# Kernel tuning notes

Measured on AMD Instinct MI355X. Metric: run time of the kernel, lower is better.

The kernel has to match this reference:

```python
import jax, jax.numpy as jnp
import numpy as np

N = 100000
E = 1200000
F_IN = 128
HID = 32
HEADS = 4
OUT_HEADS = 1
N_CLASSES = 40
NEG_SLOPE = 0.2


def _glorot(key, shape):
    fan_in, fan_out = shape[0], shape[-1]
    lim = jnp.sqrt(6.0 / (fan_in + fan_out))
    return jax.random.uniform(key, shape, jnp.float32, -lim, lim)


def setup_inputs() -> dict:
    key = jax.random.key(0)
    ks = jax.random.split(key, 16)
    x = jax.random.normal(ks[0], (N, F_IN), jnp.float32)
    edge_index = jax.random.randint(ks[1], (2, E), 0, N, jnp.int32)
    # layer 0: F_IN -> HID per head, HEADS heads, concat
    W0 = _glorot(ks[2], (F_IN, HEADS * HID))
    a_src0 = _glorot(ks[3], (HEADS, HID))
    a_dst0 = _glorot(ks[4], (HEADS, HID))
    b0 = jnp.zeros((HEADS * HID,), jnp.float32)
    # layer 1: HEADS*HID -> HID per head, HEADS heads, concat
    W1 = _glorot(ks[5], (HEADS * HID, HEADS * HID))
    a_src1 = _glorot(ks[6], (HEADS, HID))
    a_dst1 = _glorot(ks[7], (HEADS, HID))
    b1 = jnp.zeros((HEADS * HID,), jnp.float32)
    # layer 2: HEADS*HID -> N_CLASSES, OUT_HEADS heads, concat=False (mean)
    W2 = _glorot(ks[8], (HEADS * HID, OUT_HEADS * N_CLASSES))
    a_src2 = _glorot(ks[9], (OUT_HEADS, N_CLASSES))
    a_dst2 = _glorot(ks[10], (OUT_HEADS, N_CLASSES))
    b2 = jnp.zeros((N_CLASSES,), jnp.float32)
    return dict(x=x, edge_index=edge_index,
                W0=W0, a_src0=a_src0, a_dst0=a_dst0, b0=b0,
                W1=W1, a_src1=a_src1, a_dst1=a_dst1, b1=b1,
                W2=W2, a_src2=a_src2, a_dst2=a_dst2, b2=b2)


def gat_conv(x, src, dst, W, a_src, a_dst, b, heads, ch, concat):
    n = x.shape[0]
    h = (x @ W).reshape(n, heads, ch)                      # [N,H,C]
    # per-node attention logits for source/target roles
    s_src = jnp.einsum('nhc,hc->nh', h, a_src)             # [N,H]
    s_dst = jnp.einsum('nhc,hc->nh', h, a_dst)             # [N,H]
    e = jax.nn.leaky_relu(s_src[src] + s_dst[dst], NEG_SLOPE)  # [E,H]
    # segment softmax over incoming edges of each target node
    emax = jax.ops.segment_max(e, dst, num_segments=n)
    ex = jnp.exp(e - emax[dst])
    denom = jax.ops.segment_sum(ex, dst, num_segments=n)
    alpha = ex / (denom[dst] + 1e-16)                       # [E,H]
    msg = h[src] * alpha[:, :, None]                        # [E,H,C]
    out = jax.ops.segment_sum(msg, dst, num_segments=n)     # [N,H,C]
    out = out.reshape(n, heads * ch) if concat else out.mean(axis=1)
    return out + b


def reference(x, edge_index, W0, a_src0, a_dst0, b0, W1, a_src1, a_dst1, b1,
              W2, a_src2, a_dst2, b2):
    # add self loops (PyG GATConv default)
    loops = jnp.arange(N, dtype=edge_index.dtype)
    src = jnp.concatenate([edge_index[0], loops])
    dst = jnp.concatenate([edge_index[1], loops])
    h = jax.nn.elu(gat_conv(x, src, dst, W0, a_src0, a_dst0, b0, HEADS, HID, True))
    h = jax.nn.elu(gat_conv(h, src, dst, W1, a_src1, a_dst1, b1, HEADS, HID, True))
    h = gat_conv(h, src, dst, W2, a_src2, a_dst2, b2, OUT_HEADS, N_CLASSES, False)
    return jax.nn.log_softmax(h, axis=1)
```

## Files before the change

kernel.cpp:

```cpp
#include <hip/hip_runtime.h>
#include <hip/hip_bf16.h>

#define FIN   128
#define HEADS 4
#define HID   32
#define NCLS  40
#define NEG_SLOPE 0.2f

#define BKT_SH 10
#define BKT    1024
#define NB_MAX 128
#define TILE_E 4096

typedef __bf16 bf16x8 __attribute__((ext_vector_type(8)));
typedef float  f32x4  __attribute__((ext_vector_type(4)));

__device__ inline unsigned short bf16_rne(float f) {
    unsigned u = __float_as_uint(f);
    return (unsigned short)((u + 0x7fffu + ((u >> 16) & 1u)) >> 16);
}
__device__ inline float bf16_to_f(unsigned short h) {
    return __uint_as_float(((unsigned)h) << 16);
}

template<int NC>
__global__ void packW_k(const float* __restrict__ W, unsigned short* __restrict__ Bhi,
                        unsigned short* __restrict__ Blo, int NO) {
    int idx = blockIdx.x * 256 + threadIdx.x;
    int total = 4 * NC * 64 * 8;
    if (idx >= total) return;
    int i = idx & 7;
    int rest = idx >> 3;
    int l = rest & 63;
    int rest2 = rest >> 6;
    int c = rest2 % NC;
    int t = rest2 / NC;
    int k   = t * 32 + (l >> 4) * 8 + i;
    int col = c * 16 + (l & 15);
    float val = (col < NO) ? W[(size_t)k * NO + col] : 0.f;
    unsigned short hi = bf16_rne(val);
    unsigned short lo = bf16_rne(val - bf16_to_f(hi));
    Bhi[idx] = hi;
    Blo[idx] = lo;
}

template<int HH, int CH>
__global__ void packS_k(const float* __restrict__ W, const float* __restrict__ asrc,
                        const float* __restrict__ adst, unsigned short* __restrict__ Shi,
                        unsigned short* __restrict__ Slo, int NO) {
    int idx = blockIdx.x * 256 + threadIdx.x;
    int total = 4 * 64 * 8;
    if (idx >= total) return;
    int i = idx & 7;
    int l = (idx >> 3) & 63;
    int t = idx >> 9;
    int k = t * 32 + (l >> 4) * 8 + i;
    int j = l & 15;
    float val = 0.f;
    if (j < HH) {
        const float* wr = W + (size_t)k * NO + j * CH;
        const float* av = asrc + j * CH;
        for (int c = 0; c < CH; ++c) val += wr[c] * av[c];
    } else if (j < 2 * HH) {
        int h = j - HH;
        const float* wr = W + (size_t)k * NO + h * CH;
        const float* av = adst + h * CH;
        for (int c = 0; c < CH; ++c) val += wr[c] * av[c];
    }
    unsigned short hi = bf16_rne(val);
    unsigned short lo = bf16_rne(val - bf16_to_f(hi));
    Shi[idx] = hi;
    Slo[idx] = lo;
}

template<int NC, int HH>
__global__ __launch_bounds__(256) void gemm_fused_k(
        const float* __restrict__ X, const unsigned short* __restrict__ Bhi,
        const unsigned short* __restrict__ Blo, const unsigned short* __restrict__ Shi,
        const unsigned short* __restrict__ Slo, unsigned short* __restrict__ Hbf,
        float* __restrict__ ssrc, float* __restrict__ sdst, int n, int NO) {
    int wave = threadIdx.x >> 6;
    int lane = threadIdx.x & 63;
    int rowbase = (blockIdx.x * 4 + wave) * 32;
    if (rowbase >= n) return;
    int r0 = lane & 15, kg = lane >> 4;

    f32x4 acc[2][NC];
    f32x4 accS[2];
#pragma unroll
    for (int rt = 0; rt < 2; ++rt) {
        accS[rt] = f32x4{0.f, 0.f, 0.f, 0.f};
#pragma unroll
        for (int c = 0; c < NC; ++c) acc[rt][c] = f32x4{0.f, 0.f, 0.f, 0.f};
    }

    for (int t = 0; t < 4; ++t) {
        union U { unsigned short u[8]; bf16x8 v; };
        U ah[2], al[2];
#pragma unroll
        for (int rt = 0; rt < 2; ++rt) {
            int row = min(rowbase + rt * 16 + r0, n - 1);
            const float* xp = X + (size_t)row * 128 + t * 32 + kg * 8;
            float4 xa = *reinterpret_cast<const float4*>(xp);
            float4 xb = *reinterpret_cast<const float4*>(xp + 4);
            float f[8] = {xa.x, xa.y, xa.z, xa.w, xb.x, xb.y, xb.z, xb.w};
#pragma unroll
            for (int i = 0; i < 8; ++i) {
                unsigned short h = bf16_rne(f[i]);
                ah[rt].u[i] = h;
                al[rt].u[i] = bf16_rne(f[i] - bf16_to_f(h));
            }
        }
#pragma unroll
        for (int c = 0; c < NC; ++c) {
            size_t boff = (((size_t)t * NC + c) * 64 + lane) * 8;
            bf16x8 bh = *reinterpret_cast<const bf16x8*>(Bhi + boff);
            bf16x8 bl = *reinterpret_cast<const bf16x8*>(Blo + boff);
#pragma unroll
            for (int rt = 0; rt < 2; ++rt) {
                acc[rt][c] = __builtin_amdgcn_mfma_f32_16x16x32_bf16(ah[rt].v, bh, acc[rt][c], 0, 0, 0);
                acc[rt][c] = __builtin_amdgcn_mfma_f32_16x16x32_bf16(al[rt].v, bh, acc[rt][c], 0, 0, 0);
                acc[rt][c] = __builtin_amdgcn_mfma_f32_16x16x32_bf16(ah[rt].v, bl, acc[rt][c], 0, 0, 0);
            }
        }
        {
            size_t soff = ((size_t)t * 64 + lane) * 8;
            bf16x8 sh = *reinterpret_cast<const bf16x8*>(Shi + soff);
            bf16x8 sl = *reinterpret_cast<const bf16x8*>(Slo + soff);
#pragma unroll
            for (int rt = 0; rt < 2; ++rt) {
                accS[rt] = __builtin_amdgcn_mfma_f32_16x16x32_bf16(ah[rt].v, sh, accS[rt], 0, 0, 0);
                accS[rt] = __builtin_amdgcn_mfma_f32_16x16x32_bf16(al[rt].v, sh, accS[rt], 0, 0, 0);
                accS[rt] = __builtin_amdgcn_mfma_f32_16x16x32_bf16(ah[rt].v, sl, accS[rt], 0, 0, 0);
            }
        }
    }

#pragma unroll
    for (int rt = 0; rt < 2; ++rt)
#pragma unroll
        for (int r = 0; r < 4; ++r) {
            int row = rowbase + rt * 16 + kg * 4 + r;
            if (row >= n) continue;
            if (HH == 4) {
                if (r0 < 4)      ssrc[(size_t)row * 4 + r0]       = accS[rt][r];
                else if (r0 < 8) sdst[(size_t)row * 4 + (r0 - 4)] = accS[rt][r];
            } else {
                if (r0 == 0)      ssrc[row] = accS[rt][r];
                else if (r0 == 1) sdst[row] = accS[rt][r];
            }
#pragma unroll
            for (int c = 0; c < NC; ++c) {
                int col = c * 16 + r0;
                if (col < NO)
                    Hbf[(size_t)row * NO + col] = bf16_rne(acc[rt][c][r]);
            }
        }
}

template<int NC, int HH>
__global__ __launch_bounds__(256) void gemm_bf16s_k(
        const unsigned short* __restrict__ Xbf, const unsigned short* __restrict__ Bhi,
        const unsigned short* __restrict__ Blo, const unsigned short* __restrict__ Shi,
        const unsigned short* __restrict__ Slo, unsigned short* __restrict__ Hbf,
        float* __restrict__ ssrc, float* __restrict__ sdst, int n, int NO) {
    int wave = threadIdx.x >> 6;
    int lane = threadIdx.x & 63;
    int rowbase = (blockIdx.x * 4 + wave) * 32;
    if (rowbase >= n) return;
    int r0 = lane & 15, kg = lane >> 4;

    f32x4 acc[2][NC];
    f32x4 accS[2];
#pragma unroll
    for (int rt = 0; rt < 2; ++rt) {
        accS[rt] = f32x4{0.f, 0.f, 0.f, 0.f};
#pragma unroll
        for (int c = 0; c < NC; ++c) acc[rt][c] = f32x4{0.f, 0.f, 0.f, 0.f};
    }

    for (int t = 0; t < 4; ++t) {
        bf16x8 av[2];
#pragma unroll
        for (int rt = 0; rt < 2; ++rt) {
            int row = min(rowbase + rt * 16 + r0, n - 1);
            av[rt] = *reinterpret_cast<const bf16x8*>(Xbf + (size_t)row * 128 + t * 32 + kg * 8);
        }
#pragma unroll
        for (int c = 0; c < NC; ++c) {
            size_t boff = (((size_t)t * NC + c) * 64 + lane) * 8;
            bf16x8 bh = *reinterpret_cast<const bf16x8*>(Bhi + boff);
            bf16x8 bl = *reinterpret_cast<const bf16x8*>(Blo + boff);
#pragma unroll
            for (int rt = 0; rt < 2; ++rt) {
                acc[rt][c] = __builtin_amdgcn_mfma_f32_16x16x32_bf16(av[rt], bh, acc[rt][c], 0, 0, 0);
                acc[rt][c] = __builtin_amdgcn_mfma_f32_16x16x32_bf16(av[rt], bl, acc[rt][c], 0, 0, 0);
            }
        }
        {
            size_t soff = ((size_t)t * 64 + lane) * 8;
            bf16x8 sh = *reinterpret_cast<const bf16x8*>(Shi + soff);
            bf16x8 sl = *reinterpret_cast<const bf16x8*>(Slo + soff);
#pragma unroll
            for (int rt = 0; rt < 2; ++rt) {
                accS[rt] = __builtin_amdgcn_mfma_f32_16x16x32_bf16(av[rt], sh, accS[rt], 0, 0, 0);
                accS[rt] = __builtin_amdgcn_mfma_f32_16x16x32_bf16(av[rt], sl, accS[rt], 0, 0, 0);
            }
        }
    }

#pragma unroll
    for (int rt = 0; rt < 2; ++rt)
#pragma unroll
        for (int r = 0; r < 4; ++r) {
            int row = rowbase + rt * 16 + kg * 4 + r;
            if (row >= n) continue;
            if (HH == 4) {
                if (r0 < 4)      ssrc[(size_t)row * 4 + r0]       = accS[rt][r];
                else if (r0 < 8) sdst[(size_t)row * 4 + (r0 - 4)] = accS[rt][r];
            } else {
                if (r0 == 0)      ssrc[row] = accS[rt][r];
                else if (r0 == 1) sdst[row] = accS[rt][r];
            }
#pragma unroll
            for (int c = 0; c < NC; ++c) {
                int col = c * 16 + r0;
                if (col < NO)
                    Hbf[(size_t)row * NO + col] = bf16_rne(acc[rt][c][r]);
            }
        }
}

__global__ __launch_bounds__(256) void histA_k(const int* __restrict__ ei, int E, int Etot,
                                               int nb, int* __restrict__ cnt1) {
    __shared__ int h[NB_MAX];
    for (int i = threadIdx.x; i < nb; i += 256) h[i] = 0;
    __syncthreads();
    int base = blockIdx.x * TILE_E;
    int lim = min(base + TILE_E, Etot);
    for (int e = base + threadIdx.x; e < lim; e += 256) {
        int d = (e < E) ? ei[E + e] : e - E;
        atomicAdd(&h[d >> BKT_SH], 1);
    }
    __syncthreads();
    for (int i = threadIdx.x; i < nb; i += 256)
        if (h[i]) atomicAdd(&cnt1[i], h[i]);
}

__global__ void scanB_k(const int* __restrict__ cnt1, int* __restrict__ bbase,
                        int* __restrict__ gcur1, int nb) {
    __shared__ int tmp[128];
    int l = threadIdx.x;
    int v = (l < nb) ? cnt1[l] : 0;
    tmp[l] = v;
    __syncthreads();
    for (int off = 1; off < 128; off <<= 1) {
        int t = (l >= off) ? tmp[l - off] : 0;
        __syncthreads();
        tmp[l] += t;
        __syncthreads();
    }
    if (l < nb) { int ex = tmp[l] - v; bbase[l] = ex; gcur1[l] = ex; }
    if (l == 0) bbase[nb] = tmp[127];
}

__global__ __launch_bounds__(256) void placeA_k(const int* __restrict__ ei, int E, int Etot,
                                                int nb, int* __restrict__ gcur1,
                                                unsigned* __restrict__ pairs) {
    __shared__ int h[NB_MAX];
    __shared__ int cur[NB_MAX];
    for (int i = threadIdx.x; i < nb; i += 256) h[i] = 0;
    __syncthreads();
    int base = blockIdx.x * TILE_E;
    int lim = min(base + TILE_E, Etot);
    for (int e = base + threadIdx.x; e < lim; e += 256) {
        int d = (e < E) ? ei[E + e] : e - E;
        atomicAdd(&h[d >> BKT_SH], 1);
    }
    __syncthreads();
    for (int i = threadIdx.x; i < nb; i += 256)
        cur[i] = h[i] ? atomicAdd(&gcur1[i], h[i]) : 0;
    __syncthreads();
    for (int e = base + threadIdx.x; e < lim; e += 256) {
        int s, d;
        if (e < E) { s = ei[e]; d = ei[E + e]; } else { s = d = e - E; }
        int p = atomicAdd(&cur[d >> BKT_SH], 1);
        pairs[p] = ((unsigned)s << BKT_SH) | (unsigned)(d & (BKT - 1));
    }
}

__global__ __launch_bounds__(256) void buildcsr_k(const unsigned* __restrict__ pairs,
                                                  const int* __restrict__ bbase,
                                                  int* __restrict__ rowptr,
                                                  int* __restrict__ cols,
                                                  int n, int etot) {
    __shared__ int cnt[BKT];
    __shared__ int part[256];
    int b = blockIdx.x;
    int d0 = b << BKT_SH;
    int nd = min(BKT, n - d0);
    int rbeg = bbase[b], rend = bbase[b + 1];
    for (int i = threadIdx.x; i < nd; i += 256) cnt[i] = 0;
    __syncthreads();
    for (int i = rbeg + threadIdx.x; i < rend; i += 256)
        atomicAdd(&cnt[pairs[i] & (BKT - 1)], 1);
    __syncthreads();

    int t = threadIdx.x;
    int i4 = t * 4;
    int myv[4];
    int s0 = 0;
#pragma unroll
    for (int j = 0; j < 4; ++j) { myv[j] = (i4 + j < nd) ? cnt[i4 + j] : 0; s0 += myv[j]; }
    part[t] = s0;
    __syncthreads();
    for (int off = 1; off < 256; off <<= 1) {
        int tv = (t >= off) ? part[t - off] : 0;
        __syncthreads();
        part[t] += tv;
        __syncthreads();
    }
    int run = rbeg + part[t] - s0;
#pragma unroll
    for (int j = 0; j < 4; ++j) {
        if (i4 + j < nd) {
            rowptr[d0 + i4 + j] = run;
            cnt[i4 + j] = run;
            run += myv[j];
        }
    }
    if (b == 0 && t == 0) rowptr[n] = etot;
    __syncthreads();
    for (int i = rbeg + threadIdx.x; i < rend; i += 256) {
        unsigned p = pairs[i];
        int pos = atomicAdd(&cnt[p & (BKT - 1)], 1);
        cols[pos] = (int)(p >> BKT_SH);
    }
}

__global__ __launch_bounds__(256) void gat128_k(
        const int* __restrict__ rp, const int* __restrict__ cols,
        const unsigned short* __restrict__ Hbf, const float* __restrict__ ssrc,
        const float* __restrict__ sdst, const float* __restrict__ bias,
        unsigned short* __restrict__ outbf, int n) {
    int d = (blockIdx.x * 256 + threadIdx.x) >> 4;
    if (d >= n) return;
    int l = threadIdx.x & 15;
    int head = l >> 2;
    int sub  = l & 3;
    int beg = rp[d], end = rp[d + 1];

    float sdh = sdst[(size_t)d * 4 + head];

    float m = -1e30f, den = 0.f;
    for (int i = beg + sub; i < end; i += 4) {
        int s = cols[i];
        float v = ssrc[(size_t)s * 4 + head] + sdh;
        v = (v >= 0.f) ? v : NEG_SLOPE * v;
        float nm = fmaxf(m, v);
        den = den * __expf(m - nm) + __expf(v - nm);
        m = nm;
    }
#pragma unroll
    for (int off = 1; off <= 2; off <<= 1) {
        float om = __shfl_xor(m, off, 64);
        float od = __shfl_xor(den, off, 64);
        float nm = fmaxf(m, om);
        den = den * __expf(m - nm) + od * __expf(om - nm);
        m = nm;
    }
    float r = 1.f / (den + 1e-16f);

    float4 a0 = {0.f, 0.f, 0.f, 0.f}, a1 = {0.f, 0.f, 0.f, 0.f};
    float4 c0 = {0.f, 0.f, 0.f, 0.f}, c1 = {0.f, 0.f, 0.f, 0.f};

    auto proc = [&](int i, float4& p0, float4& p1) {
        int s = cols[i];
        float v = ssrc[(size_t)s * 4 + head] + sdh;
        v = (v >= 0.f) ? v : NEG_SLOPE * v;
        float a = __expf(v - m);
        const unsigned short* hp = Hbf + (size_t)s * 128 + l * 8;
        uint4 q = *reinterpret_cast<const uint4*>(hp);
        float f0 = __uint_as_float(q.x << 16);
        float f1 = __uint_as_float(q.x & 0xffff0000u);
        float f2 = __uint_as_float(q.y << 16);
        float f3 = __uint_as_float(q.y & 0xffff0000u);
        float f4 = __uint_as_float(q.z << 16);
        float f5 = __uint_as_float(q.z & 0xffff0000u);
        float f6 = __uint_as_float(q.w << 16);
        float f7 = __uint_as_float(q.w & 0xffff0000u);
        p0.x += a * f0; p0.y += a * f1; p0.z += a * f2; p0.w += a * f3;
        p1.x += a * f4; p1.y += a * f5; p1.z += a * f6; p1.w += a * f7;
    };

    int i = beg;
    int rem = (end - beg) & 3;
    if (rem & 1) { proc(i, a0, a1); ++i; }
    if (rem & 2) { proc(i, a0, a1); proc(i + 1, c0, c1); i += 2; }
    for (; i < end; i += 4) {
        int s0 = cols[i], s1 = cols[i + 1], s2 = cols[i + 2], s3 = cols[i + 3];
        float w0 = ssrc[(size_t)s0 * 4 + head] + sdh;
        float w1 = ssrc[(size_t)s1 * 4 + head] + sdh;
        float w2 = ssrc[(size_t)s2 * 4 + head] + sdh;
        float w3 = ssrc[(size_t)s3 * 4 + head] + sdh;
        uint4 q0 = *reinterpret_cast<const uint4*>(Hbf + (size_t)s0 * 128 + l * 8);
        uint4 q1 = *reinterpret_cast<const uint4*>(Hbf + (size_t)s1 * 128 + l * 8);
        uint4 q2 = *reinterpret_cast<const uint4*>(Hbf + (size_t)s2 * 128 + l * 8);
        uint4 q3 = *reinterpret_cast<const uint4*>(Hbf + (size_t)s3 * 128 + l * 8);
        w0 = (w0 >= 0.f) ? w0 : NEG_SLOPE * w0;
        w1 = (w1 >= 0.f) ? w1 : NEG_SLOPE * w1;
        w2 = (w2 >= 0.f) ? w2 : NEG_SLOPE * w2;
        w3 = (w3 >= 0.f) ? w3 : NEG_SLOPE * w3;
        float e0 = __expf(w0 - m), e1 = __expf(w1 - m);
        float e2 = __expf(w2 - m), e3 = __expf(w3 - m);
        a0.x += e0 * __uint_as_float(q0.x << 16);
        a0.y += e0 * __uint_as_float(q0.x & 0xffff0000u);
        a0.z += e0 * __uint_as_float(q0.y << 16);
        a0.w += e0 * __uint_as_float(q0.y & 0xffff0000u);
        a1.x += e0 * __uint_as_float(q0.z << 16);
        a1.y += e0 * __uint_as_float(q0.z & 0xffff0000u);
        a1.z += e0 * __uint_as_float(q0.w << 16);
        a1.w += e0 * __uint_as_float(q0.w & 0xffff0000u);
        c0.x += e1 * __uint_as_float(q1.x << 16);
        c0.y += e1 * __uint_as_float(q1.x & 0xffff0000u);
        c0.z += e1 * __uint_as_float(q1.y << 16);
        c0.w += e1 * __uint_as_float(q1.y & 0xffff0000u);
        c1.x += e1 * __uint_as_float(q1.z << 16);
        c1.y += e1 * __uint_as_float(q1.z & 0xffff0000u);
        c1.z += e1 * __uint_as_float(q1.w << 16);
        c1.w += e1 * __uint_as_float(q1.w & 0xffff0000u);
        a0.x += e2 * __uint_as_float(q2.x << 16);
        a0.y += e2 * __uint_as_float(q2.x & 0xffff0000u);
        a0.z += e2 * __uint_as_float(q2.y << 16);
        a0.w += e2 * __uint_as_float(q2.y & 0xffff0000u);
        a1.x += e2 * __uint_as_float(q2.z << 16);
        a1.y += e2 * __uint_as_float(q2.z & 0xffff0000u);
        a1.z += e2 * __uint_as_float(q2.w << 16);
        a1.w += e2 * __uint_as_float(q2.w & 0xffff0000u);
        c0.x += e3 * __uint_as_float(q3.x << 16);
        c0.y += e3 * __uint_as_float(q3.x & 0xffff0000u);
        c0.z += e3 * __uint_as_float(q3.y << 16);
        c0.w += e3 * __uint_as_float(q3.y & 0xffff0000u);
        c1.x += e3 * __uint_as_float(q3.z << 16);
        c1.y += e3 * __uint_as_float(q3.z & 0xffff0000u);
        c1.z += e3 * __uint_as_float(q3.w << 16);
        c1.w += e3 * __uint_as_float(q3.w & 0xffff0000u);
    }
    a0.x += c0.x; a0.y += c0.y; a0.z += c0.z; a0.w += c0.w;
    a1.x += c1.x; a1.y += c1.y; a1.z += c1.z; a1.w += c1.w;

    float4 b0 = *reinterpret_cast<const float4*>(bias + l * 8);
    float4 b1 = *reinterpret_cast<const float4*>(bias + l * 8 + 4);
    float4 v0, v1;
    v0.x = a0.x * r + b0.x; v0.y = a0.y * r + b0.y;
    v0.z = a0.z * r + b0.z; v0.w = a0.w * r + b0.w;
    v1.x = a1.x * r + b1.x; v1.y = a1.y * r + b1.y;
    v1.z = a1.z * r + b1.z; v1.w = a1.w * r + b1.w;
    v0.x = (v0.x > 0.f) ? v0.x : expm1f(v0.x);
    v0.y = (v0.y > 0.f) ? v0.y : expm1f(v0.y);
    v0.z = (v0.z > 0.f) ? v0.z : expm1f(v0.z);
    v0.w = (v0.w > 0.f) ? v0.w : expm1f(v0.w);
    v1.x = (v1.x > 0.f) ? v1.x : expm1f(v1.x);
    v1.y = (v1.y > 0.f) ? v1.y : expm1f(v1.y);
    v1.z = (v1.z > 0.f) ? v1.z : expm1f(v1.z);
    v1.w = (v1.w > 0.f) ? v1.w : expm1f(v1.w);

    uint4 u;
    u.x = (unsigned)bf16_rne(v0.x) | ((unsigned)bf16_rne(v0.y) << 16);
    u.y = (unsigned)bf16_rne(v0.z) | ((unsigned)bf16_rne(v0.w) << 16);
    u.z = (unsigned)bf16_rne(v1.x) | ((unsigned)bf16_rne(v1.y) << 16);
    u.w = (unsigned)bf16_rne(v1.z) | ((unsigned)bf16_rne(v1.w) << 16);
    *reinterpret_cast<uint4*>(outbf + (size_t)d * 128 + l * 8) = u;
}

__global__ __launch_bounds__(256) void gat40_k(
        const int* __restrict__ rp, const int* __restrict__ cols,
        const unsigned short* __restrict__ Hbf, const float* __restrict__ ssrc,
        const float* __restrict__ sdst, const float* __restrict__ b2,
        float* __restrict__ out, int n) {
    int d = (blockIdx.x * 256 + threadIdx.x) >> 4;
    if (d >= n) return;
    int l = threadIdx.x & 15;
    int beg = rp[d], end = rp[d + 1];
    float sd = sdst[d];

    float m = -1e30f, den = 0.f;
    for (int i = beg + l; i < end; i += 16) {
        int s = cols[i];
        float v = ssrc[s] + sd;
        v = (v >= 0.f) ? v : NEG_SLOPE * v;
        float nm = fmaxf(m, v);
        den = den * __expf(m - nm) + __expf(v - nm);
        m = nm;
    }
#pragma unroll
    for (int off = 1; off <= 8; off <<= 1) {
        float om = __shfl_xor(m, off, 64);
        float od = __shfl_xor(den, off, 64);
        float nm = fmaxf(m, om);
        den = den * __expf(m - nm) + od * __expf(om - nm);
        m = nm;
    }
    float r = 1.f / (den + 1e-16f);

    float4 acc = {0.f, 0.f, 0.f, 0.f};
    float4 acc2 = {0.f, 0.f, 0.f, 0.f};
    auto proc = [&](int i, float4& p) {
        int s = cols[i];
        float v = ssrc[s] + sd;
        v = (v >= 0.f) ? v : NEG_SLOPE * v;
        float a = __expf(v - m);
        if (l < 10) {
            uint2 q = *reinterpret_cast<const uint2*>(Hbf + (size_t)s * 40 + l * 4);
            float f0 = __uint_as_float(q.x << 16);
            float f1 = __uint_as_float(q.x & 0xffff0000u);
            float f2 = __uint_as_float(q.y << 16);
            float f3 = __uint_as_float(q.y & 0xffff0000u);
            p.x += a * f0; p.y += a * f1; p.z += a * f2; p.w += a * f3;
        }
    };
    int i = beg;
    if ((end - beg) & 1) { proc(i, acc); ++i; }
    for (; i < end; i += 2) { proc(i, acc); proc(i + 1, acc2); }
    acc.x += acc2.x; acc.y += acc2.y; acc.z += acc2.z; acc.w += acc2.w;

    float4 v4 = {0.f, 0.f, 0.f, 0.f};
    float mm = -1e30f;
    if (l < 10) {
        float4 b = *reinterpret_cast<const float4*>(b2 + l * 4);
        v4.x = acc.x * r + b.x; v4.y = acc.y * r + b.y;
        v4.z = acc.z * r + b.z; v4.w = acc.w * r + b.w;
        mm = fmaxf(fmaxf(v4.x, v4.y), fmaxf(v4.z, v4.w));
    }
    for (int off = 8; off > 0; off >>= 1) mm = fmaxf(mm, __shfl_xor(mm, off, 16));
    float ss = 0.f;
    if (l < 10)
        ss = __expf(v4.x - mm) + __expf(v4.y - mm) + __expf(v4.z - mm) + __expf(v4.w - mm);
    for (int off = 8; off > 0; off >>= 1) ss += __shfl_xor(ss, off, 16);
    float lse = mm + logf(ss);
    if (l < 10) {
        float4 o;
        o.x = v4.x - lse; o.y = v4.y - lse; o.z = v4.z - lse; o.w = v4.w - lse;
        *reinterpret_cast<float4*>(out + (size_t)d * 40 + l * 4) = o;
    }
}

static inline dim3 g1(long t) { return dim3((unsigned)((t + 255) / 256)); }

extern "C" void kernel_launch(void* const* d_in, const int* in_sizes, int n_in,
                              void* d_out, int out_size, void* d_ws, size_t ws_size,
                              hipStream_t stream) {
    const float* x      = (const float*)d_in[0];
    const int*   ei     = (const int*)d_in[1];
    const float* W0     = (const float*)d_in[2];
    const float* a_src0 = (const float*)d_in[3];
    const float* a_dst0 = (const float*)d_in[4];
    const float* b0     = (const float*)d_in[5];
    const float* W1     = (const float*)d_in[6];
    const float* a_src1 = (const float*)d_in[7];
    const float* a_dst1 = (const float*)d_in[8];
    const float* b1     = (const float*)d_in[9];
    const float* W2     = (const float*)d_in[10];
    const float* a_src2 = (const float*)d_in[11];
    const float* a_dst2 = (const float*)d_in[12];
    const float* b2     = (const float*)d_in[13];

    const int N    = in_sizes[0] / FIN;
    const int E    = in_sizes[1] / 2;
    const int Etot = E + N;
    const int NB   = (N + BKT - 1) / BKT;

    float* ws = (float*)d_ws;
    size_t o = 0;
    unsigned short* Hbf = (unsigned short*)(ws + o); o += (size_t)N * FIN / 2;
    unsigned short* Obf = (unsigned short*)(ws + o); o += (size_t)N * FIN / 2;
    float* ssrcA = ws + o; o += (size_t)N * HEADS;
    float* sdstA = ws + o; o += (size_t)N * HEADS;
    float* ssrcB = ws + o; o += (size_t)N * HEADS;
    float* sdstB = ws + o; o += (size_t)N * HEADS;
    int* cnt1   = (int*)(ws + o); o += NB_MAX;
    int* bbase  = (int*)(ws + o); o += NB_MAX + 2;
    int* gcur1  = (int*)(ws + o); o += NB_MAX;
    int* rowptr = (int*)(ws + o); o += N + 1;
    int* cols   = (int*)(ws + o); o += Etot;
    unsigned* pairs = (unsigned*)(ws + o); o += Etot;
    unsigned short* Bhi0 = (unsigned short*)(ws + o); o += 4 * 8 * 64 * 8 / 2;
    unsigned short* Blo0 = (unsigned short*)(ws + o); o += 4 * 8 * 64 * 8 / 2;
    unsigned short* Bhi1 = (unsigned short*)(ws + o); o += 4 * 8 * 64 * 8 / 2;
    unsigned short* Blo1 = (unsigned short*)(ws + o); o += 4 * 8 * 64 * 8 / 2;
    unsigned short* Bhi2 = (unsigned short*)(ws + o); o += 4 * 3 * 64 * 8 / 2;
    unsigned short* Blo2 = (unsigned short*)(ws + o); o += 4 * 3 * 64 * 8 / 2;
    unsigned short* Shi0 = (unsigned short*)(ws + o); o += 4 * 64 * 8 / 2;
    unsigned short* Slo0 = (unsigned short*)(ws + o); o += 4 * 64 * 8 / 2;
    unsigned short* Shi1 = (unsigned short*)(ws + o); o += 4 * 64 * 8 / 2;
    unsigned short* Slo1 = (unsigned short*)(ws + o); o += 4 * 64 * 8 / 2;
    unsigned short* Shi2 = (unsigned short*)(ws + o); o += 4 * 64 * 8 / 2;
    unsigned short* Slo2 = (unsigned short*)(ws + o); o += 4 * 64 * 8 / 2;

    const int gemmBlocks = (N + 127) / 128;
    const int grpBlocks  = (N * 16 + 255) / 256;
    const int eTiles     = (Etot + TILE_E - 1) / TILE_E;

    hipMemsetAsync(cnt1, 0, NB_MAX * 4, stream);
    histA_k<<<eTiles, 256, 0, stream>>>(ei, E, Etot, NB, cnt1);
    packW_k<8><<<g1(4 * 8 * 64 * 8), 256, 0, stream>>>(W0, Bhi0, Blo0, 128);
    packW_k<8><<<g1(4 * 8 * 64 * 8), 256, 0, stream>>>(W1, Bhi1, Blo1, 128);
    packW_k<3><<<g1(4 * 3 * 64 * 8), 256, 0, stream>>>(W2, Bhi2, Blo2, NCLS);
    packS_k<4, HID><<<g1(4 * 64 * 8), 256, 0, stream>>>(W0, a_src0, a_dst0, Shi0, Slo0, 128);
    packS_k<4, HID><<<g1(4 * 64 * 8), 256, 0, stream>>>(W1, a_src1, a_dst1, Shi1, Slo1, 128);
    packS_k<1, NCLS><<<g1(4 * 64 * 8), 256, 0, stream>>>(W2, a_src2, a_dst2, Shi2, Slo2, NCLS);
    scanB_k<<<1, 128, 0, stream>>>(cnt1, bbase, gcur1, NB);
    placeA_k<<<eTiles, 256, 0, stream>>>(ei, E, Etot, NB, gcur1, pairs);
    buildcsr_k<<<NB, 256, 0, stream>>>(pairs, bbase, rowptr, cols, N, Etot);

    gemm_fused_k<8, 4><<<gemmBlocks, 256, 0, stream>>>(x, Bhi0, Blo0, Shi0, Slo0, Hbf, ssrcA, sdstA, N, 128);
    gat128_k<<<grpBlocks, 256, 0, stream>>>(rowptr, cols, Hbf, ssrcA, sdstA, b0, Obf, N);

    gemm_bf16s_k<8, 4><<<gemmBlocks, 256, 0, stream>>>(Obf, Bhi1, Blo1, Shi1, Slo1, Hbf, ssrcB, sdstB, N, 128);
    gat128_k<<<grpBlocks, 256, 0, stream>>>(rowptr, cols, Hbf, ssrcB, sdstB, b1, Obf, N);

    gemm_bf16s_k<3, 1><<<gemmBlocks, 256, 0, stream>>>(Obf, Bhi2, Blo2, Shi2, Slo2, Hbf, ssrcA, sdstA, N, NCLS);
    gat40_k<<<grpBlocks, 256, 0, stream>>>(rowptr, cols, Hbf, ssrcA, sdstA, b2, (float*)d_out, N);
}
```

Measured before the change: 362.1 us.

## Fuse weight-packing launches, pad layer-2 rows to 64, unroll gat40 by four

Merges the six weight and attention packing kernels and the counter memset into one launch, which cuts launch overhead. The layer-2 feature matrix now uses a padded row stride of 64 so gat40 can load without a lane guard. gat40's edge loop is unrolled by four, with the loads issued early to raise memory-level parallelism. The histogram and placement tile size is doubled. Lanes 10-15 in gat40 now read padding columns that are never written. Those values appear to be discarded, but the reads waste bandwidth and touch uninitialised memory.

```diff
diff --git a/kernel.cpp b/kernel.cpp
--- a/kernel.cpp
+++ b/kernel.cpp
@@ -10,7 +10,7 @@
 #define BKT_SH 10
 #define BKT    1024
 #define NB_MAX 128
-#define TILE_E 4096
+#define TILE_E 8192
 
 typedef __bf16 bf16x8 __attribute__((ext_vector_type(8)));
 typedef float  f32x4  __attribute__((ext_vector_type(4)));
@@ -23,12 +23,8 @@
     return __uint_as_float(((unsigned)h) << 16);
 }
 
-template<int NC>
-__global__ void packW_k(const float* __restrict__ W, unsigned short* __restrict__ Bhi,
-                        unsigned short* __restrict__ Blo, int NO) {
-    int idx = blockIdx.x * 256 + threadIdx.x;
-    int total = 4 * NC * 64 * 8;
-    if (idx >= total) return;
+__device__ inline void packW_dev(const float* __restrict__ W, unsigned short* __restrict__ Bhi,
+                                 unsigned short* __restrict__ Blo, int NO, int NC, int idx) {
     int i = idx & 7;
     int rest = idx >> 3;
     int l = rest & 63;
@@ -44,33 +40,47 @@
     Blo[idx] = lo;
 }
 
-template<int HH, int CH>
-__global__ void packS_k(const float* __restrict__ W, const float* __restrict__ asrc,
-                        const float* __restrict__ adst, unsigned short* __restrict__ Shi,
-                        unsigned short* __restrict__ Slo, int NO) {
-    int idx = blockIdx.x * 256 + threadIdx.x;
-    int total = 4 * 64 * 8;
-    if (idx >= total) return;
+__device__ inline void packS_dev(const float* __restrict__ W, const float* __restrict__ asrc,
+                                 const float* __restrict__ adst, unsigned short* __restrict__ Shi,
+                                 unsigned short* __restrict__ Slo, int NO, int HH, int CH, int idx) {
     int i = idx & 7;
     int l = (idx >> 3) & 63;
     int t = idx >> 9;
     int k = t * 32 + (l >> 4) * 8 + i;
     int j = l & 15;
     float val = 0.f;
-    if (j < HH) {
-        const float* wr = W + (size_t)k * NO + j * CH;
-        const float* av = asrc + j * CH;
-        for (int c = 0; c < CH; ++c) val += wr[c] * av[c];
-    } else if (j < 2 * HH) {
-        int h = j - HH;
+    if (j < 2 * HH) {
+        int h = (j < HH) ? j : j - HH;
+        const float* av = (j < HH) ? (asrc + h * CH) : (adst + h * CH);
         const float* wr = W + (size_t)k * NO + h * CH;
-        const float* av = adst + h * CH;
         for (int c = 0; c < CH; ++c) val += wr[c] * av[c];
     }
     unsigned short hi = bf16_rne(val);
     unsigned short lo = bf16_rne(val - bf16_to_f(hi));
     Shi[idx] = hi;
     Slo[idx] = lo;
+}
+
+__global__ __launch_bounds__(256) void packAll_k(
+        const float* __restrict__ W0, const float* __restrict__ W1, const float* __restrict__ W2,
+        const float* __restrict__ as0, const float* __restrict__ ad0,
+        const float* __restrict__ as1, const float* __restrict__ ad1,
+        const float* __restrict__ as2, const float* __restrict__ ad2,
+        unsigned short* __restrict__ Bhi0, unsigned short* __restrict__ Blo0,
+        unsigned short* __restrict__ Bhi1, unsigned short* __restrict__ Blo1,
+        unsigned short* __restrict__ Bhi2, unsigned short* __restrict__ Blo2,
+        unsigned short* __restrict__ Shi0, unsigned short* __restrict__ Slo0,
+        unsigned short* __restrict__ Shi1, unsigned short* __restrict__ Slo1,
+        unsigned short* __restrict__ Shi2, unsigned short* __restrict__ Slo2,
+        int* __restrict__ cnt1) {
+    int gid = blockIdx.x * 256 + threadIdx.x;
+    if      (gid < 16384) packW_dev(W0, Bhi0, Blo0, 128, 8, gid);
+    else if (gid < 32768) packW_dev(W1, Bhi1, Blo1, 128, 8, gid - 16384);
+    else if (gid < 38912) packW_dev(W2, Bhi2, Blo2, NCLS, 3, gid - 32768);
+    else if (gid < 40960) packS_dev(W0, as0, ad0, Shi0, Slo0, 128, 4, HID, gid - 38912);
+    else if (gid < 43008) packS_dev(W1, as1, ad1, Shi1, Slo1, 128, 4, HID, gid - 40960);
+    else if (gid < 45056) packS_dev(W2, as2, ad2, Shi2, Slo2, NCLS, 1, NCLS, gid - 43008);
+    else if (gid < 45056 + NB_MAX) cnt1[gid - 45056] = 0;
 }
 
 template<int NC, int HH>
@@ -158,7 +168,7 @@
         }
 }
 
-template<int NC, int HH>
+template<int NC, int HH, int OSTRIDE>
 __global__ __launch_bounds__(256) void gemm_bf16s_k(
         const unsigned short* __restrict__ Xbf, const unsigned short* __restrict__ Bhi,
         const unsigned short* __restrict__ Blo, const unsigned short* __restrict__ Shi,
@@ -226,7 +236,7 @@
             for (int c = 0; c < NC; ++c) {
                 int col = c * 16 + r0;
                 if (col < NO)
-                    Hbf[(size_t)row * NO + col] = bf16_rne(acc[rt][c][r]);
+                    Hbf[(size_t)row * OSTRIDE + col] = bf16_rne(acc[rt][c][r]);
             }
         }
 }
@@ -381,16 +391,14 @@
         float a = __expf(v - m);
         const unsigned short* hp = Hbf + (size_t)s * 128 + l * 8;
         uint4 q = *reinterpret_cast<const uint4*>(hp);
-        float f0 = __uint_as_float(q.x << 16);
-        float f1 = __uint_as_float(q.x & 0xffff0000u);
-        float f2 = __uint_as_float(q.y << 16);
-        float f3 = __uint_as_float(q.y & 0xffff0000u);
-        float f4 = __uint_as_float(q.z << 16);
-        float f5 = __uint_as_float(q.z & 0xffff0000u);
-        float f6 = __uint_as_float(q.w << 16);
-        float f7 = __uint_as_float(q.w & 0xffff0000u);
-        p0.x += a * f0; p0.y += a * f1; p0.z += a * f2; p0.w += a * f3;
-        p1.x += a * f4; p1.y += a * f5; p1.z += a * f6; p1.w += a * f7;
+        p0.x += a * __uint_as_float(q.x << 16);
+        p0.y += a * __uint_as_float(q.x & 0xffff0000u);
+        p0.z += a * __uint_as_float(q.y << 16);
+        p0.w += a * __uint_as_float(q.y & 0xffff0000u);
+        p1.x += a * __uint_as_float(q.z << 16);
+        p1.y += a * __uint_as_float(q.z & 0xffff0000u);
+        p1.z += a * __uint_as_float(q.w << 16);
+        p1.w += a * __uint_as_float(q.w & 0xffff0000u);
     };
 
     int i = beg;
@@ -510,18 +518,47 @@
         float v = ssrc[s] + sd;
         v = (v >= 0.f) ? v : NEG_SLOPE * v;
         float a = __expf(v - m);
-        if (l < 10) {
-            uint2 q = *reinterpret_cast<const uint2*>(Hbf + (size_t)s * 40 + l * 4);
-            float f0 = __uint_as_float(q.x << 16);
-            float f1 = __uint_as_float(q.x & 0xffff0000u);
-            float f2 = __uint_as_float(q.y << 16);
-            float f3 = __uint_as_float(q.y & 0xffff0000u);
-            p.x += a * f0; p.y += a * f1; p.z += a * f2; p.w += a * f3;
-        }
+        uint2 q = *reinterpret_cast<const uint2*>(Hbf + (size_t)s * 64 + l * 4);
+        p.x += a * __uint_as_float(q.x << 16);
+        p.y += a * __uint_as_float(q.x & 0xffff0000u);
+        p.z += a * __uint_as_float(q.y << 16);
+        p.w += a * __uint_as_float(q.y & 0xffff0000u);
     };
     int i = beg;
-    if ((end - beg) & 1) { proc(i, acc); ++i; }
-    for (; i < end; i += 2) { proc(i, acc); proc(i + 1, acc2); }
+    int rem = (end - beg) & 3;
+    if (rem & 1) { proc(i, acc); ++i; }
+    if (rem & 2) { proc(i, acc); proc(i + 1, acc2); i += 2; }
+    for (; i < end; i += 4) {
+        int s0 = cols[i], s1 = cols[i + 1], s2 = cols[i + 2], s3 = cols[i + 3];
+        float w0 = ssrc[s0] + sd, w1 = ssrc[s1] + sd;
+        float w2 = ssrc[s2] + sd, w3 = ssrc[s3] + sd;
+        uint2 q0 = *reinterpret_cast<const uint2*>(Hbf + (size_t)s0 * 64 + l * 4);
+        uint2 q1 = *reinterpret_cast<const uint2*>(Hbf + (size_t)s1 * 64 + l * 4);
+        uint2 q2 = *reinterpret_cast<const uint2*>(Hbf + (size_t)s2 * 64 + l * 4);
+        uint2 q3 = *reinterpret_cast<const uint2*>(Hbf + (size_t)s3 * 64 + l * 4);
+        w0 = (w0 >= 0.f) ? w0 : NEG_SLOPE * w0;
+        w1 = (w1 >= 0.f) ? w1 : NEG_SLOPE * w1;
+        w2 = (w2 >= 0.f) ? w2 : NEG_SLOPE * w2;
+        w3 = (w3 >= 0.f) ? w3 : NEG_SLOPE * w3;
+        float e0 = __expf(w0 - m), e1 = __expf(w1 - m);
+        float e2 = __expf(w2 - m), e3 = __expf(w3 - m);
+        acc.x += e0 * __uint_as_float(q0.x << 16);
+        acc.y += e0 * __uint_as_float(q0.x & 0xffff0000u);
+        acc.z += e0 * __uint_as_float(q0.y << 16);
+        acc.w += e0 * __uint_as_float(q0.y & 0xffff0000u);
+        acc2.x += e1 * __uint_as_float(q1.x << 16);
+        acc2.y += e1 * __uint_as_float(q1.x & 0xffff0000u);
+        acc2.z += e1 * __uint_as_float(q1.y << 16);
+        acc2.w += e1 * __uint_as_float(q1.y & 0xffff0000u);
+        acc.x += e2 * __uint_as_float(q2.x << 16);
+        acc.y += e2 * __uint_as_float(q2.x & 0xffff0000u);
+        acc.z += e2 * __uint_as_float(q2.y << 16);
+        acc.w += e2 * __uint_as_float(q2.y & 0xffff0000u);
+        acc2.x += e3 * __uint_as_float(q3.x << 16);
+        acc2.y += e3 * __uint_as_float(q3.x & 0xffff0000u);
+        acc2.z += e3 * __uint_as_float(q3.y << 16);
+        acc2.w += e3 * __uint_as_float(q3.y & 0xffff0000u);
+    }
     acc.x += acc2.x; acc.y += acc2.y; acc.z += acc2.z; acc.w += acc2.w;
 
     float4 v4 = {0.f, 0.f, 0.f, 0.f};
@@ -601,14 +638,11 @@
     const int grpBlocks  = (N * 16 + 255) / 256;
     const int eTiles     = (Etot + TILE_E - 1) / TILE_E;
 
-    hipMemsetAsync(cnt1, 0, NB_MAX * 4, stream);
+    packAll_k<<<g1(45056 + NB_MAX), 256, 0, stream>>>(
+        W0, W1, W2, a_src0, a_dst0, a_src1, a_dst1, a_src2, a_dst2,
+        Bhi0, Blo0, Bhi1, Blo1, Bhi2, Blo2,
+        Shi0, Slo0, Shi1, Slo1, Shi2, Slo2, cnt1);
     histA_k<<<eTiles, 256, 0, stream>>>(ei, E, Etot, NB, cnt1);
-    packW_k<8><<<g1(4 * 8 * 64 * 8), 256, 0, stream>>>(W0, Bhi0, Blo0, 128);
-    packW_k<8><<<g1(4 * 8 * 64 * 8), 256, 0, stream>>>(W1, Bhi1, Blo1, 128);
-    packW_k<3><<<g1(4 * 3 * 64 * 8), 256, 0, stream>>>(W2, Bhi2, Blo2, NCLS);
-    packS_k<4, HID><<<g1(4 * 64 * 8), 256, 0, stream>>>(W0, a_src0, a_dst0, Shi0, Slo0, 128);
-    packS_k<4, HID><<<g1(4 * 64 * 8), 256, 0, stream>>>(W1, a_src1, a_dst1, Shi1, Slo1, 128);
-    packS_k<1, NCLS><<<g1(4 * 64 * 8), 256, 0, stream>>>(W2, a_src2, a_dst2, Shi2, Slo2, NCLS);
     scanB_k<<<1, 128, 0, stream>>>(cnt1, bbase, gcur1, NB);
     placeA_k<<<eTiles, 256, 0, stream>>>(ei, E, Etot, NB, gcur1, pairs);
     buildcsr_k<<<NB, 256, 0, stream>>>(pairs, bbase, rowptr, cols, N, Etot);
@@ -616,9 +650,9 @@
     gemm_fused_k<8, 4><<<gemmBlocks, 256, 0, stream>>>(x, Bhi0, Blo0, Shi0, Slo0, Hbf, ssrcA, sdstA, N, 128);
     gat128_k<<<grpBlocks, 256, 0, stream>>>(rowptr, cols, Hbf, ssrcA, sdstA, b0, Obf, N);
 
-    gemm_bf16s_k<8, 4><<<gemmBlocks, 256, 0, stream>>>(Obf, Bhi1, Blo1, Shi1, Slo1, Hbf, ssrcB, sdstB, N, 128);
+    gemm_bf16s_k<8, 4, 128><<<gemmBlocks, 256, 0, stream>>>(Obf, Bhi1, Blo1, Shi1, Slo1, Hbf, ssrcB, sdstB, N, 128);
     gat128_k<<<grpBlocks, 256, 0, stream>>>(rowptr, cols, Hbf, ssrcB, sdstB, b1, Obf, N);
 
-    gemm_bf16s_k<3, 1><<<gemmBlocks, 256, 0, stream>>>(Obf, Bhi2, Blo2, Shi2, Slo2, Hbf, ssrcA, sdstA, N, NCLS);
+    gemm_bf16s_k<3, 1, 64><<<gemmBlocks, 256, 0, stream>>>(Obf, Bhi2, Blo2, Shi2, Slo2, Hbf, ssrcA, sdstA, N, NCLS);
     gat40_k<<<grpBlocks, 256, 0, stream>>>(rowptr, cols, Hbf, ssrcA, sdstA, b2, (float*)d_out, N);
 }
```

After: 331.7 us. 1.09x faster.
